# Optimization experiments

Measured on AMD Instinct MI355X. Metric: run time of the kernel, lower is better.

## Reference

```python
import jax, jax.numpy as jnp
import numpy as np
from itertools import product

SPATIAL1 = (41, 1600, 1408)  # (z,y,x) = grid[::-1] + [1,0,0]
NUM_BATCH = 2
BN_EPS = 1e-3

# ---------- numpy rulebook construction (spconv-style, done once on host) ----------

def _encode(c, shape):
    D, H, W = [int(v) for v in shape]
    return ((c[:, 0].astype(np.int64) * D + c[:, 1]) * H + c[:, 2]) * W + c[:, 3]

def _lookup(skeys, order, cand):
    pos = np.clip(np.searchsorted(skeys, cand), 0, len(skeys) - 1)
    hit = skeys[pos] == cand
    return hit, order[pos]

def _pad_rb(pairs, n_in, n_out):
    P = max(max(len(a) for a, _ in pairs), 1)
    K = len(pairs)
    ii = np.full((K, P), n_in, np.int32)   # sentinel -> zero feature row
    oo = np.full((K, P), n_out, np.int32)  # sentinel -> dummy output row
    for k, (a, b) in enumerate(pairs):
        ii[k, :len(a)] = a
        oo[k, :len(b)] = b
    return ii, oo

def _subm_rb(coords, shape):
    # SubMConv3d k=3 p=1 s=1: output sites == input sites
    N = len(coords)
    keys = _encode(coords, shape)
    order = np.argsort(keys); skeys = keys[order]
    dims = np.array(shape)
    pairs = []
    for off in product((-1, 0, 1), repeat=3):
        nb = coords[:, 1:] + np.array(off)
        ok = (nb >= 0).all(1) & (nb < dims).all(1)
        oid = np.nonzero(ok)[0]
        cand = _encode(np.concatenate([coords[ok, :1], nb[ok]], 1), shape)
        hit, iid = _lookup(skeys, order, cand)
        pairs.append((iid[hit].astype(np.int32), oid[hit].astype(np.int32)))
    return _pad_rb(pairs, N, N)

def _down_rb(coords, in_shape, ks, st, pd):
    # SparseConv3d: output site active iff any kernel tap hits an active input
    dims = np.array(in_shape); ks = np.array(ks); st = np.array(st); pd = np.array(pd)
    out_shape = (dims + 2 * pd - ks) // st + 1
    offs = list(product(*[range(int(k)) for k in ks]))
    outs = []
    for off in offs:
        o = coords[:, 1:] + pd - np.array(off)
        ok = (o % st == 0).all(1)
        od = o // st
        ok &= (od >= 0).all(1) & (od < out_shape).all(1)
        outs.append(np.concatenate([coords[ok, :1], od[ok]], 1))
    out_coords = np.unique(np.concatenate(outs, 0), axis=0)
    keys = _encode(coords, in_shape)
    order = np.argsort(keys); skeys = keys[order]
    pairs = []
    for off in offs:
        ic = out_coords[:, 1:] * st - pd + np.array(off)
        ok = (ic >= 0).all(1) & (ic < dims).all(1)
        oid = np.nonzero(ok)[0]
        cand = _encode(np.concatenate([out_coords[ok, :1], ic[ok]], 1), in_shape)
        hit, iid = _lookup(skeys, order, cand)
        pairs.append((iid[hit].astype(np.int32), oid[hit].astype(np.int32)))
    ii, oo = _pad_rb(pairs, len(coords), len(out_coords))
    return ii, oo, out_coords, tuple(int(v) for v in out_shape)

def _gen_coords(rng):
    # clustered LiDAR-like active voxels (surfaces -> local density)
    D, H, W = SPATIAL1
    per = []
    for b in range(NUM_BATCH):
        centers = rng.integers([3, 30, 30], [D - 4, H - 31, W - 31], size=(600, 3))
        pts = centers[:, None, :] + rng.integers(-3, 4, size=(600, 60, 3))
        pts = np.clip(pts.reshape(-1, 3), 0, np.array([D - 1, H - 1, W - 1]))
        uniq = np.unique(pts, axis=0)
        per.append(np.concatenate([np.full((len(uniq), 1), b, np.int64), uniq], 1))
    return np.concatenate(per, 0)

CHANS = [(27, 4, 16), (27, 16, 16), (27, 16, 32), (27, 32, 32), (27, 32, 32),
         (27, 32, 64), (27, 64, 64), (27, 64, 64), (27, 64, 64), (27, 64, 64),
         (27, 64, 64), (3, 64, 128)]

def setup_inputs() -> dict:
    rng = np.random.default_rng(0)
    coords = _gen_coords(rng)  # (N,4) [b,z,y,x]
    N = len(coords)
    s1i, s1o = _subm_rb(coords, SPATIAL1)
    d2i, d2o, c2, s2 = _down_rb(coords, SPATIAL1, (3, 3, 3), (2, 2, 2), (1, 1, 1))
    s2i, s2o = _subm_rb(c2, s2)
    d3i, d3o, c3, s3 = _down_rb(c2, s2, (3, 3, 3), (2, 2, 2), (1, 1, 1))
    s3i, s3o = _subm_rb(c3, s3)
    d4i, d4o, c4, s4 = _down_rb(c3, s3, (3, 3, 3), (2, 2, 2), (0, 1, 1))
    s4i, s4o = _subm_rb(c4, s4)
    oi, oo, c5, s5 = _down_rb(c4, s4, (3, 1, 1), (2, 1, 1), (0, 0, 0))

    key = jax.random.key(0)
    ks = jax.random.split(key, 40)
    inp = {}
    for i, (K, ci, co) in enumerate(CHANS):
        inp[f"w{i}"] = (jax.random.normal(ks[i], (K, ci, co), jnp.float32)
                         / np.sqrt(K * ci)).astype(jnp.float32)
        kb = jax.random.split(ks[12 + i], 4)
        inp[f"bn{i}"] = jnp.stack([
            jax.random.uniform(kb[0], (co,)) + 0.5,   # gamma
            jax.random.normal(kb[1], (co,)) * 0.1,    # beta
            jax.random.normal(kb[2], (co,)) * 0.1,    # running mean
            jax.random.uniform(kb[3], (co,)) + 0.5,   # running var
        ]).astype(jnp.float32)
    inp["voxels"] = jax.random.normal(ks[30], (N, 5, 4), jnp.float32)
    inp["voxel_num_points"] = jax.random.randint(ks[31], (N,), 0, 6).astype(jnp.int32)
    for name, arr in [("subm1_in", s1i), ("subm1_out", s1o), ("down2_in", d2i),
                      ("down2_out", d2o), ("subm2_in", s2i), ("subm2_out", s2o),
                      ("down3_in", d3i), ("down3_out", d3o), ("subm3_in", s3i),
                      ("subm3_out", s3o), ("down4_in", d4i), ("down4_out", d4o),
                      ("subm4_in", s4i), ("subm4_out", s4o), ("out_in", oi),
                      ("out_out", oo)]:
        inp[name] = jnp.asarray(arr)
    inp["batch_idx"] = jnp.asarray(c5[:, 0].astype(np.int32))
    inp["n2"] = len(c2); inp["n3"] = len(c3); inp["n4"] = len(c4); inp["n5"] = len(c5)
    inp["n_batch"] = NUM_BATCH
    return inp

# ---------- jax forward ----------

def _sconv(feats, w, in_idx, out_idx, n_out):
    # gather -> per-kernel-offset GEMM -> scatter-add (spconv implicit GEMM)
    fpad = jnp.concatenate([feats, jnp.zeros((1, feats.shape[1]), feats.dtype)], 0)
    g = fpad[in_idx]                                  # (K,P,Cin)
    contrib = jnp.einsum('kpi,kio->kpo', g, w)        # (K,P,Cout)
    out = jnp.zeros((n_out + 1, w.shape[2]), feats.dtype)
    return out.at[out_idx].add(contrib)[:n_out]

def _bnrelu(x, bn):
    g, b, m, v = bn  # eval-mode BatchNorm1d, eps=1e-3
    return jax.nn.relu((x - m) * jax.lax.rsqrt(v + BN_EPS) * g + b)

def reference(voxels, voxel_num_points, w0, w1, w2, w3, w4, w5, w6, w7, w8, w9,
              w10, w11, bn0, bn1, bn2, bn3, bn4, bn5, bn6, bn7, bn8, bn9, bn10,
              bn11, subm1_in, subm1_out, down2_in, down2_out, subm2_in, subm2_out,
              down3_in, down3_out, subm3_in, subm3_out, down4_in, down4_out,
              subm4_in, subm4_out, out_in, out_out, batch_idx, n2, n3, n4, n5,
              n_batch):
    # mean-VFE: average point features per voxel
    denom = jnp.maximum(voxel_num_points.astype(voxels.dtype), 1.0)[:, None]
    x = voxels.sum(1) / denom                              # (N,4)
    n1 = x.shape[0]
    x = _bnrelu(_sconv(x, w0, subm1_in, subm1_out, n1), bn0)   # conv_input
    x = _bnrelu(_sconv(x, w1, subm1_in, subm1_out, n1), bn1)   # conv1
    x = _bnrelu(_sconv(x, w2, down2_in, down2_out, n2), bn2)   # conv2 (s2)
    x = _bnrelu(_sconv(x, w3, subm2_in, subm2_out, n2), bn3)
    x = _bnrelu(_sconv(x, w4, subm2_in, subm2_out, n2), bn4)
    x = _bnrelu(_sconv(x, w5, down3_in, down3_out, n3), bn5)   # conv3 (s2)
    x = _bnrelu(_sconv(x, w6, subm3_in, subm3_out, n3), bn6)
    x = _bnrelu(_sconv(x, w7, subm3_in, subm3_out, n3), bn7)
    x = _bnrelu(_sconv(x, w8, down4_in, down4_out, n4), bn8)   # conv4 (s2)
    x = _bnrelu(_sconv(x, w9, subm4_in, subm4_out, n4), bn9)
    x = _bnrelu(_sconv(x, w10, subm4_in, subm4_out, n4), bn10)
    x = _bnrelu(_sconv(x, w11, out_in, out_out, n5), bn11)     # conv_out
    # dc_feats: per-sample global max pool over active voxels (== max_pool1d)
    dc = jax.ops.segment_max(x, batch_idx, num_segments=n_batch)
    return dc
```

## Files before the change

kernel.cpp:

```cpp
#include <hip/hip_runtime.h>

#define TPB 256
typedef unsigned short u16;
typedef __attribute__((ext_vector_type(8))) short short8v;
typedef __attribute__((ext_vector_type(4))) float f32x4;

__device__ __forceinline__ u16 f2bf(float x) {
    unsigned u = __float_as_uint(x);
    return (u16)((u + 0x7FFFu + ((u >> 16) & 1u)) >> 16);
}
__device__ __forceinline__ float bf2f(u16 h) {
    return __uint_as_float(((unsigned)h) << 16);
}

template<int CS>
__device__ __forceinline__ int swzc(int r, int c) {
    constexpr int PH = (CS == 8) ? 0 : 1;
    return c ^ ((r >> PH) & (CS - 1));
}

__device__ __forceinline__ int xcd_swz(int bid, int nwg) {
    int q = nwg >> 3, r = nwg & 7;
    int x = bid & 7, idx = bid >> 3;
    return (x < r ? x * (q + 1) : r * (q + 1) + (x - r) * q) + idx;
}

__device__ __forceinline__ void gld16(const u16* g, u16* l) {
    __builtin_amdgcn_global_load_lds(
        (const __attribute__((address_space(1))) void*)g,
        (__attribute__((address_space(3))) void*)l, 16, 0, 0);
}

__global__ void vfe_kernel(const float* __restrict__ voxels,
                           const int* __restrict__ nump,
                           float* __restrict__ x, int N) {
    int i = blockIdx.x * blockDim.x + threadIdx.x;
    if (i >= N * 4) return;
    int n = i >> 2, c = i & 3;
    const float* v = voxels + (long)n * 20 + c;
    float s = v[0] + v[4] + v[8] + v[12] + v[16];
    x[i] = s / fmaxf((float)nump[n], 1.0f);
}

__global__ void inv_build_kernel(const int* __restrict__ rb_in,
                                 const int* __restrict__ rb_out,
                                 int* __restrict__ inv,
                                 int KP, int P, int K, int n_in) {
    int t = blockIdx.x * blockDim.x + threadIdx.x;
    if (t >= KP) return;
    int ii = rb_in[t];
    if (ii == n_in) return;
    int k = t / P;
    inv[(long)rb_out[t] * K + k] = ii;
}

struct WPE { const float* w; u16* oh; u16* ol; int K, ci, co, total; };
struct WPA { WPE e[9]; };
__global__ void wprep_kernel(WPA a, int grand) {
    int t = blockIdx.x * blockDim.x + threadIdx.x;
    if (t >= grand) return;
    #pragma unroll
    for (int i = 0; i < 9; ++i) {
        if (t < a.e[i].total) {
            const WPE& E = a.e[i];
            int cc = E.ci * E.co;
            int k = t / cc, r = t % cc, c = r / E.co, o = r % E.co;
            float x = E.w[t];
            u16 h = f2bf(x);
            float lf = x - bf2f(h);
            int cs = E.ci >> 3, ph = (cs == 8) ? 0 : 1;
            int ch = c >> 3, e = c & 7;
            int sch = ch ^ ((o >> ph) & (cs - 1));
            long d = ((long)k * E.co + o) * E.ci + sch * 8 + e;
            E.oh[d] = h; E.ol[d] = f2bf(lf);
            return;
        }
        t -= a.e[i].total;
    }
}

__global__ void wprep_paired_kernel(const float* __restrict__ w,
                                    u16* __restrict__ oh, u16* __restrict__ ol,
                                    int co, int total) {
    int t = blockIdx.x * blockDim.x + threadIdx.x;
    if (t >= total) return;
    int p = t / (co * 32);
    int rem = t % (co * 32);
    int o = rem / 32, ci = rem % 32;
    int tap = 2 * p + (ci >> 4);
    float x = (tap < 27) ? w[((long)tap * 16 + (ci & 15)) * co + o] : 0.f;
    u16 h = f2bf(x);
    float lf = x - bf2f(h);
    int ch = ci >> 3, e = ci & 7;
    int sch = ch ^ ((o >> 1) & 3);
    long d = ((long)p * co + o) * 32 + sch * 8 + e;
    oh[d] = h; ol[d] = f2bf(lf);
}

template<int CO, int K>
__global__ __launch_bounds__(256)
void dconv4_kernel(const float* __restrict__ feats,
                   const float* __restrict__ w,
                   const float* __restrict__ bn,
                   const int* __restrict__ inv,
                   u16* __restrict__ oh, u16* __restrict__ ol,
                   int n_out) {
    constexpr int OG = CO / 4;
    __shared__ float sW[K * 4 * CO];
    for (int i = threadIdx.x; i < K * 4 * CO; i += 256) sW[i] = w[i];
    __syncthreads();
    long t = (long)blockIdx.x * 256 + threadIdx.x;
    int row = (int)(t / OG), og = (int)(t % OG);
    if (row >= n_out) return;
    float a0 = 0.f, a1 = 0.f, a2 = 0.f, a3 = 0.f;
    for (int k = 0; k < K; ++k) {
        int idx = inv[(long)row * K + k];
        if (idx < 0) continue;
        float4 av = *(const float4*)(feats + (long)idx * 4);
        const float* wk = sW + k * 4 * CO + og * 4;
        #pragma unroll
        for (int ci = 0; ci < 4; ++ci) {
            float a = (&av.x)[ci];
            a0 = fmaf(a, wk[ci * CO + 0], a0);
            a1 = fmaf(a, wk[ci * CO + 1], a1);
            a2 = fmaf(a, wk[ci * CO + 2], a2);
            a3 = fmaf(a, wk[ci * CO + 3], a3);
        }
    }
    float4 g = *(const float4*)(bn + og * 4);
    float4 b = *(const float4*)(bn + CO + og * 4);
    float4 m = *(const float4*)(bn + 2 * CO + og * 4);
    float4 v = *(const float4*)(bn + 3 * CO + og * 4);
    float o4[4];
    o4[0] = fmaxf((a0 - m.x) * rsqrtf(v.x + 1e-3f) * g.x + b.x, 0.f);
    o4[1] = fmaxf((a1 - m.y) * rsqrtf(v.y + 1e-3f) * g.y + b.y, 0.f);
    o4[2] = fmaxf((a2 - m.z) * rsqrtf(v.z + 1e-3f) * g.z + b.z, 0.f);
    o4[3] = fmaxf((a3 - m.w) * rsqrtf(v.w + 1e-3f) * g.w + b.w, 0.f);
    long base = (long)row * CO + og * 4;
    #pragma unroll
    for (int c = 0; c < 4; ++c) {
        u16 h = f2bf(o4[c]);
        oh[base + c] = h;
        ol[base + c] = f2bf(o4[c] - bf2f(h));
    }
}

template<int CI, int CO, int KPt, int KT, bool PAIRED, bool DBUF, int EPI>
__global__ __launch_bounds__(256, 4)
void mconv_kernel(const u16* __restrict__ fh, const u16* __restrict__ fl,
                  const u16* __restrict__ wh, const u16* __restrict__ wl,
                  const int* __restrict__ inv,
                  const u16* __restrict__ zpage,
                  float* __restrict__ part, long slab_elems,
                  const float* __restrict__ bn,
                  u16* __restrict__ oh, u16* __restrict__ ol,
                  float* __restrict__ outf,
                  int n_out, int kpb) {
    constexpr int CS  = CI / 8;
    constexpr int LCS = (CS == 8) ? 3 : 2;
    constexpr int PH  = (CS == 8) ? 0 : 1;
    constexpr int KS  = CI / 32;
    constexpr int WC  = (CO >= 32) ? 2 : 1;
    constexpr int MT  = (WC == 2) ? 2 : 1;
    constexpr int NTW = CO / (16 * WC);
    constexpr int ASL = 64 * CS;
    constexpr int BSL = CO * CS;
    constexpr int AIT = (ASL + 255) / 256;
    constexpr int BIT = (BSL + 255) / 256;
    constexpr int NB  = DBUF ? 2 : 1;

    __shared__ __align__(16) u16 sAh[NB][64 * CI];
    __shared__ __align__(16) u16 sAl[NB][64 * CI];
    __shared__ __align__(16) u16 sBh[NB][CO * CI];
    __shared__ __align__(16) u16 sBl[NB][CO * CI];
    __shared__ int sI[64 * KT];

    const int t = threadIdx.x;
    const int bx = xcd_swz(blockIdx.x, gridDim.x);
    const int brow = bx * 64;
    const int kbeg = blockIdx.y * kpb;
    const int kend = (kbeg + kpb < KPt) ? (kbeg + kpb) : KPt;

    const int lane = t & 63, wid = t >> 6;
    const int wr = wid / WC, wc = wid % WC;
    const int frow = lane & 15;
    const int fch  = lane >> 4;

    {
        long base = (long)brow * KT, lim = (long)n_out * KT;
        for (int i = t; i < 64 * KT; i += 256)
            sI[i] = (base + i < lim) ? inv[base + i] : -1;
    }

    f32x4 acc[MT][NTW];
    #pragma unroll
    for (int mt = 0; mt < MT; ++mt)
        #pragma unroll
        for (int nt = 0; nt < NTW; ++nt) {
            acc[mt][nt][0] = 0.f; acc[mt][nt][1] = 0.f;
            acc[mt][nt][2] = 0.f; acc[mt][nt][3] = 0.f;
        }

    auto stage = [&](int b, int k) {
        #pragma unroll
        for (int s = 0; s < AIT; ++s) {
            int slot = s * 256 + t;
            if (ASL % 256 == 0 || slot < ASL) {
                int r = slot >> LCS, cc = slot & (CS - 1);
                int c = cc ^ ((r >> PH) & (CS - 1));
                const u16 *srcH, *srcL;
                if (PAIRED) {
                    int tap = 2 * k + (c >> 1);
                    int idx = (tap < KT) ? sI[r * KT + tap] : -1;
                    srcH = (idx >= 0) ? fh + (long)idx * 16 + (c & 1) * 8 : zpage;
                    srcL = (idx >= 0) ? fl + (long)idx * 16 + (c & 1) * 8 : zpage;
                } else {
                    int idx = sI[r * KT + k];
                    srcH = (idx >= 0) ? fh + (long)idx * CI + c * 8 : zpage;
                    srcL = (idx >= 0) ? fl + (long)idx * CI + c * 8 : zpage;
                }
                gld16(srcH, sAh[b] + (s * 256 + wid * 64) * 8);
                gld16(srcL, sAl[b] + (s * 256 + wid * 64) * 8);
            }
        }
        const u16* gbh = wh + (long)k * CO * CI;
        const u16* gbl = wl + (long)k * CO * CI;
        #pragma unroll
        for (int s = 0; s < BIT; ++s) {
            int slot = s * 256 + t;
            if (BSL % 256 == 0 || slot < BSL) {
                gld16(gbh + (long)slot * 8, sBh[b] + (s * 256 + wid * 64) * 8);
                gld16(gbl + (long)slot * 8, sBl[b] + (s * 256 + wid * 64) * 8);
            }
        }
    };
    auto compute = [&](int b) {
        #pragma unroll
        for (int ks = 0; ks < KS; ++ks) {
            int c = ks * 4 + fch;
            short8v ah[MT], al[MT];
            #pragma unroll
            for (int mt = 0; mt < MT; ++mt) {
                int r = wr * (MT * 16) + mt * 16 + frow;
                int o = r * CI + swzc<CS>(r, c) * 8;
                ah[mt] = *(const short8v*)(sAh[b] + o);
                al[mt] = *(const short8v*)(sAl[b] + o);
            }
            #pragma unroll
            for (int nt = 0; nt < NTW; ++nt) {
                int col = wc * (CO / WC) + nt * 16 + frow;
                int o = col * CI + swzc<CS>(col, c) * 8;
                short8v bh = *(const short8v*)(sBh[b] + o);
                short8v bl = *(const short8v*)(sBl[b] + o);
                #pragma unroll
                for (int mt = 0; mt < MT; ++mt) {
                    acc[mt][nt] = __builtin_amdgcn_mfma_f32_16x16x32_bf16(ah[mt], bh, acc[mt][nt], 0, 0, 0);
                    acc[mt][nt] = __builtin_amdgcn_mfma_f32_16x16x32_bf16(ah[mt], bl, acc[mt][nt], 0, 0, 0);
                    acc[mt][nt] = __builtin_amdgcn_mfma_f32_16x16x32_bf16(al[mt], bh, acc[mt][nt], 0, 0, 0);
                }
            }
        }
    };

    __syncthreads();
    if (DBUF) {
        stage(0, kbeg);
        int cur = 0;
        for (int k = kbeg; k < kend; ++k) {
            __syncthreads();
            if (k + 1 < kend) stage(cur ^ 1, k + 1);
            compute(cur);
            cur ^= 1;
        }
    } else {
        for (int k = kbeg; k < kend; ++k) {
            stage(0, k);
            __syncthreads();
            compute(0);
            if (k + 1 < kend) __syncthreads();
        }
    }

    if constexpr (EPI == 0) {
        float* dst = part + (long)blockIdx.y * slab_elems;
        #pragma unroll
        for (int mt = 0; mt < MT; ++mt) {
            int orow0 = brow + wr * (MT * 16) + mt * 16 + (lane >> 4) * 4;
            #pragma unroll
            for (int nt = 0; nt < NTW; ++nt) {
                int ocol = wc * (CO / WC) + nt * 16 + (lane & 15);
                #pragma unroll
                for (int j = 0; j < 4; ++j) {
                    int r = orow0 + j;
                    if (r < n_out) dst[(long)r * CO + ocol] = acc[mt][nt][j];
                }
            }
        }
    } else {
        #pragma unroll
        for (int mt = 0; mt < MT; ++mt) {
            int orow0 = brow + wr * (MT * 16) + mt * 16 + (lane >> 4) * 4;
            #pragma unroll
            for (int nt = 0; nt < NTW; ++nt) {
                int ocol = wc * (CO / WC) + nt * 16 + (lane & 15);
                float g = bn[ocol], bb = bn[CO + ocol];
                float m = bn[2 * CO + ocol], vv = bn[3 * CO + ocol];
                float sc = rsqrtf(vv + 1e-3f) * g;
                #pragma unroll
                for (int j = 0; j < 4; ++j) {
                    int r = orow0 + j;
                    if (r < n_out) {
                        float yv = fmaxf((acc[mt][nt][j] - m) * sc + bb, 0.f);
                        if constexpr (EPI == 1) {
                            u16 h = f2bf(yv);
                            oh[(long)r * CO + ocol] = h;
                            ol[(long)r * CO + ocol] = f2bf(yv - bf2f(h));
                        } else {
                            outf[(long)r * CO + ocol] = yv;
                        }
                    }
                }
            }
        }
    }
}

template<bool EMIT16>
__global__ void reduce_bnrelu_kernel(const float* __restrict__ part, long stride,
                                     int ys, const float* __restrict__ bn, int co,
                                     float* __restrict__ outf,
                                     u16* __restrict__ oh, u16* __restrict__ ol,
                                     long total) {
    long t = (long)blockIdx.x * blockDim.x + threadIdx.x;
    if (t >= total) return;
    float s = 0.f;
    for (int y = 0; y < ys; ++y) s += part[(long)y * stride + t];
    int o = (int)(t % co);
    float g = bn[o], b = bn[co + o], m = bn[2 * co + o], v = bn[3 * co + o];
    float yv = fmaxf((s - m) * rsqrtf(v + 1e-3f) * g + b, 0.f);
    if (EMIT16) {
        u16 h = f2bf(yv);
        oh[t] = h;
        ol[t] = f2bf(yv - bf2f(h));
    } else {
        outf[t] = yv;
    }
}

__global__ void segmax_kernel(const float* __restrict__ x,
                              const int* __restrict__ bidx,
                              float* __restrict__ out, int rows, int nb) {
    __shared__ float sM[8 * 128];
    for (int i = threadIdx.x; i < nb * 128; i += 256) sM[i] = 0.f;
    __syncthreads();
    int c = threadIdx.x & 127;
    int sub = threadIdx.x >> 7;
    for (int r = blockIdx.x * 2 + sub; r < rows; r += gridDim.x * 2) {
        float v = x[(long)r * 128 + c];
        int b = bidx[r];
        atomicMax((int*)&sM[b * 128 + c], __float_as_int(v));
    }
    __syncthreads();
    for (int i = threadIdx.x; i < nb * 128; i += 256)
        atomicMax((int*)out + i, __float_as_int(sM[i]));
}

extern "C" void kernel_launch(void* const* d_in, const int* in_sizes, int n_in,
                              void* d_out, int out_size, void* d_ws, size_t ws_size,
                              hipStream_t stream) {
    (void)n_in;
    const float* voxels = (const float*)d_in[24];
    const int*   nump   = (const int*)d_in[25];
    const int N  = in_sizes[25];
    const int n2 = in_sizes[30] / 27;
    const int n3 = in_sizes[34] / 27;
    const int n4 = in_sizes[38] / 27;
    const int n5 = in_sizes[42];

    struct L { int wi, rb, K, ci, co, nin, nout; };
    const L layers[12] = {
        {0,  26, 27,  4,  16, N,  N }, {1,  26, 27, 16,  16, N,  N },
        {2,  28, 27, 16,  32, N,  n2}, {3,  30, 27, 32,  32, n2, n2},
        {4,  30, 27, 32,  32, n2, n2}, {5,  32, 27, 32,  64, n2, n3},
        {6,  34, 27, 64,  64, n3, n3}, {7,  34, 27, 64,  64, n3, n3},
        {8,  36, 27, 64,  64, n3, n4}, {9,  38, 27, 64,  64, n4, n4},
        {10, 38, 27, 64,  64, n4, n4}, {11, 40,  3, 64, 128, n4, n5},
    };
    struct RBD { int rb, K, nin, nout; };
    const RBD rbs[8] = {
        {26, 27, N,  N }, {28, 27, N,  n2}, {30, 27, n2, n2}, {32, 27, n2, n3},
        {34, 27, n3, n3}, {36, 27, n3, n4}, {38, 27, n4, n4}, {40, 3,  n4, n5},
    };
    const int invmap[12] = {0, 0, 1, 2, 2, 3, 4, 4, 5, 6, 6, 7};

    size_t feat_elems = (size_t)N * 4, wt_elems = 0, arena_elems = 0;
    for (int i = 0; i < 12; ++i) {
        size_t fe = (size_t)layers[i].nout * layers[i].co;
        if (fe > feat_elems) feat_elems = fe;
        if (i >= 3) wt_elems += (size_t)layers[i].K * layers[i].ci * layers[i].co;
    }
    for (int r = 0; r < 8; ++r) arena_elems += (size_t)rbs[r].nout * rbs[r].K;
    const size_t wp1_elems = 14 * 32 * 16;
    const size_t wp2_elems = 14 * 32 * 32;
    auto al = [](size_t x) { return (x + 255) & ~(size_t)255; };
    char* p = (char*)d_ws;
    u16*   zpage = (u16*)p; p += 256;
    int*   inv_arena = (int*)p; p += al(arena_elems * 4);
    float* bufA = (float*)p; p += al(feat_elems * 4);
    u16* ph[2]; u16* pl[2];
    ph[0] = (u16*)p; p += al(feat_elems * 2);
    pl[0] = (u16*)p; p += al(feat_elems * 2);
    ph[1] = (u16*)p; p += al(feat_elems * 2);
    pl[1] = (u16*)p; p += al(feat_elems * 2);
    u16* wth = (u16*)p; p += al(wt_elems * 2);
    u16* wtl = (u16*)p; p += al(wt_elems * 2);
    u16* wp1h = (u16*)p; p += al(wp1_elems * 2);
    u16* wp1l = (u16*)p; p += al(wp1_elems * 2);
    u16* wp2h = (u16*)p; p += al(wp2_elems * 2);
    u16* wp2l = (u16*)p; p += al(wp2_elems * 2);
    float* slab = (float*)p;
    size_t slab_budget = ws_size - (size_t)((char*)slab - (char*)d_ws);

    hipMemsetAsync(zpage, 0, 256, stream);

    int* invs[8];
    {
        size_t off = 0;
        for (int r = 0; r < 8; ++r) { invs[r] = inv_arena + off; off += (size_t)rbs[r].nout * rbs[r].K; }
        hipMemsetAsync(inv_arena, 0xFF, arena_elems * sizeof(int), stream);
        for (int r = 0; r < 8; ++r) {
            const int* rin  = (const int*)d_in[rbs[r].rb];
            const int* rout = (const int*)d_in[rbs[r].rb + 1];
            int P  = in_sizes[rbs[r].rb] / rbs[r].K;
            int KP = rbs[r].K * P;
            inv_build_kernel<<<dim3((KP + TPB - 1) / TPB), dim3(TPB), 0, stream>>>(
                rin, rout, invs[r], KP, P, rbs[r].K, rbs[r].nin);
        }
    }

    {
        long tot = (long)N * 4;
        vfe_kernel<<<dim3((unsigned)((tot + TPB - 1) / TPB)), dim3(TPB), 0, stream>>>(
            voxels, nump, bufA, N);
    }

    size_t woff[9];
    {
        WPA wa;
        size_t off = 0;
        for (int i = 0; i < 9; ++i) {
            const L& l = layers[i + 3];
            woff[i] = off;
            wa.e[i].w  = (const float*)d_in[2 * l.wi];
            wa.e[i].oh = wth + off;
            wa.e[i].ol = wtl + off;
            wa.e[i].K = l.K; wa.e[i].ci = l.ci; wa.e[i].co = l.co;
            wa.e[i].total = l.K * l.ci * l.co;
            off += (size_t)wa.e[i].total;
        }
        int grand = (int)off;
        wprep_kernel<<<dim3((grand + TPB - 1) / TPB), dim3(TPB), 0, stream>>>(wa, grand);
        wprep_paired_kernel<<<dim3(((int)wp1_elems + TPB - 1) / TPB), dim3(TPB), 0, stream>>>(
            (const float*)d_in[2], wp1h, wp1l, 16, (int)wp1_elems);
        wprep_paired_kernel<<<dim3(((int)wp2_elems + TPB - 1) / TPB), dim3(TPB), 0, stream>>>(
            (const float*)d_in[4], wp2h, wp2l, 32, (int)wp2_elems);
    }

    {
        const L& l = layers[0];
        long tot = (long)l.nout * 4;
        dconv4_kernel<16, 27><<<dim3((unsigned)((tot + 255) / 256)), 256, 0, stream>>>(
            bufA, (const float*)d_in[0], (const float*)d_in[1], invs[0],
            ph[0], pl[0], l.nout);
    }

    int cset = 0;
    for (int i = 1; i < 12; ++i) {
        const L& l = layers[i];
        const int* invp = invs[invmap[i]];
        unsigned blocks = (unsigned)((l.nout + 63) / 64);
        int KPv = (i <= 2) ? 14 : l.K;
        int ysmax = (KPv == 14) ? 9 : ((KPv == 27) ? 27 : 3);
        size_t per = (size_t)l.nout * l.co * 4;
        int ys = 1;
        while (ys < ysmax && blocks * (unsigned)ys < 768) ys *= 3;
        if (ys > ysmax) ys = ysmax;
        while (ys > 1 && (size_t)ys * per > slab_budget) ys /= 3;
        int kpb = (KPv + ys - 1) / ys;
        long slab_elems = (long)l.nout * l.co;
        dim3 grid(blocks, (unsigned)ys);
        const float* bn = (const float*)d_in[2 * l.wi + 1];
        const u16* fh = ph[cset];
        const u16* fl = pl[cset];
        const u16* whp = (i >= 3) ? wth + woff[i - 3] : nullptr;
        const u16* wlp = (i >= 3) ? wtl + woff[i - 3] : nullptr;

        #define MCONV(CI_, CO_, KP_, KT_, PRD_, WH_, WL_)                              \
            do {                                                                       \
                if (ys == 1 && i < 11)                                                 \
                    mconv_kernel<CI_, CO_, KP_, KT_, PRD_, true, 1><<<grid, 256, 0, stream>>>( \
                        fh, fl, WH_, WL_, invp, zpage, nullptr, 0, bn,                 \
                        ph[cset ^ 1], pl[cset ^ 1], nullptr, l.nout, kpb);             \
                else if (ys == 1)                                                      \
                    mconv_kernel<CI_, CO_, KP_, KT_, PRD_, true, 2><<<grid, 256, 0, stream>>>( \
                        fh, fl, WH_, WL_, invp, zpage, nullptr, 0, bn,                 \
                        nullptr, nullptr, bufA, l.nout, kpb);                          \
                else if (kpb >= 2)                                                     \
                    mconv_kernel<CI_, CO_, KP_, KT_, PRD_, true, 0><<<grid, 256, 0, stream>>>( \
                        fh, fl, WH_, WL_, invp, zpage, slab, slab_elems, bn,           \
                        nullptr, nullptr, nullptr, l.nout, kpb);                       \
                else                                                                   \
                    mconv_kernel<CI_, CO_, KP_, KT_, PRD_, false, 0><<<grid, 256, 0, stream>>>( \
                        fh, fl, WH_, WL_, invp, zpage, slab, slab_elems, bn,           \
                        nullptr, nullptr, nullptr, l.nout, kpb);                       \
            } while (0)

        switch (i) {
        case 1:          MCONV(32, 16, 14, 27, true,  wp1h, wp1l); break;
        case 2:          MCONV(32, 32, 14, 27, true,  wp2h, wp2l); break;
        case 3: case 4:  MCONV(32, 32, 27, 27, false, whp, wlp);   break;
        case 5:          MCONV(32, 64, 27, 27, false, whp, wlp);   break;
        case 11:         MCONV(64, 128, 3, 3,  false, whp, wlp);   break;
        default:         MCONV(64, 64, 27, 27, false, whp, wlp);   break;
        }
        #undef MCONV

        if (ys == 1) {
            if (i < 11) cset ^= 1;
        } else {
            long total = (long)l.nout * l.co;
            unsigned rblocks = (unsigned)((total + TPB - 1) / TPB);
            if (i < 11) {
                reduce_bnrelu_kernel<true><<<dim3(rblocks), dim3(TPB), 0, stream>>>(
                    slab, slab_elems, ys, bn, l.co,
                    nullptr, ph[cset ^ 1], pl[cset ^ 1], total);
                cset ^= 1;
            } else {
                reduce_bnrelu_kernel<false><<<dim3(rblocks), dim3(TPB), 0, stream>>>(
                    slab, slab_elems, ys, bn, l.co, bufA, nullptr, nullptr, total);
            }
        }
    }

    hipMemsetAsync(d_out, 0, (size_t)out_size * sizeof(float), stream);
    const int* bidx = (const int*)d_in[42];
    int nb = out_size / 128;
    segmax_kernel<<<dim3(128), dim3(256), 0, stream>>>(bufA, bidx, (float*)d_out, n5, nb);
}
```

Baseline: 482.6 us.

## Drop double-buffered staging and shared index cache in sparse conv kernel

Removes the double-buffered shared-memory pipeline and the per-block shared copy of the rulebook indices. Each tap is now staged, synced and computed in sequence, and the gather reads indices straight from global memory. The aim is to halve LDS use so more blocks fit per CU and to drop the up-front index preload. The cost is that loads for the next tap no longer overlap compute, and index reads become dependent global loads on the gather path.

```diff
diff --git a/kernel.cpp b/kernel.cpp
--- a/kernel.cpp
+++ b/kernel.cpp
@@ -145,7 +145,7 @@
     }
 }
 
-template<int CI, int CO, int KPt, int KT, bool PAIRED, bool DBUF, int EPI>
+template<int CI, int CO, int KPt, int KT, bool PAIRED, int EPI>
 __global__ __launch_bounds__(256, 4)
 void mconv_kernel(const u16* __restrict__ fh, const u16* __restrict__ fl,
                   const u16* __restrict__ wh, const u16* __restrict__ wl,
@@ -167,13 +167,11 @@
     constexpr int BSL = CO * CS;
     constexpr int AIT = (ASL + 255) / 256;
     constexpr int BIT = (BSL + 255) / 256;
-    constexpr int NB  = DBUF ? 2 : 1;
-
-    __shared__ __align__(16) u16 sAh[NB][64 * CI];
-    __shared__ __align__(16) u16 sAl[NB][64 * CI];
-    __shared__ __align__(16) u16 sBh[NB][CO * CI];
-    __shared__ __align__(16) u16 sBl[NB][CO * CI];
-    __shared__ int sI[64 * KT];
+
+    __shared__ __align__(16) u16 sAh[64 * CI];
+    __shared__ __align__(16) u16 sAl[64 * CI];
+    __shared__ __align__(16) u16 sBh[CO * CI];
+    __shared__ __align__(16) u16 sBl[CO * CI];
 
     const int t = threadIdx.x;
     const int bx = xcd_swz(blockIdx.x, gridDim.x);
@@ -186,12 +184,6 @@
     const int frow = lane & 15;
     const int fch  = lane >> 4;
 
-    {
-        long base = (long)brow * KT, lim = (long)n_out * KT;
-        for (int i = t; i < 64 * KT; i += 256)
-            sI[i] = (base + i < lim) ? inv[base + i] : -1;
-    }
-
     f32x4 acc[MT][NTW];
     #pragma unroll
     for (int mt = 0; mt < MT; ++mt)
@@ -201,26 +193,28 @@
             acc[mt][nt][2] = 0.f; acc[mt][nt][3] = 0.f;
         }
 
-    auto stage = [&](int b, int k) {
+    auto stage = [&](int k) {
         #pragma unroll
         for (int s = 0; s < AIT; ++s) {
             int slot = s * 256 + t;
             if (ASL % 256 == 0 || slot < ASL) {
                 int r = slot >> LCS, cc = slot & (CS - 1);
                 int c = cc ^ ((r >> PH) & (CS - 1));
+                int grow = brow + r;
                 const u16 *srcH, *srcL;
                 if (PAIRED) {
                     int tap = 2 * k + (c >> 1);
-                    int idx = (tap < KT) ? sI[r * KT + tap] : -1;
+                    int idx = (grow < n_out && tap < KT)
+                              ? inv[(long)grow * KT + tap] : -1;
                     srcH = (idx >= 0) ? fh + (long)idx * 16 + (c & 1) * 8 : zpage;
                     srcL = (idx >= 0) ? fl + (long)idx * 16 + (c & 1) * 8 : zpage;
                 } else {
-                    int idx = sI[r * KT + k];
+                    int idx = (grow < n_out) ? inv[(long)grow * KT + k] : -1;
                     srcH = (idx >= 0) ? fh + (long)idx * CI + c * 8 : zpage;
                     srcL = (idx >= 0) ? fl + (long)idx * CI + c * 8 : zpage;
                 }
-                gld16(srcH, sAh[b] + (s * 256 + wid * 64) * 8);
-                gld16(srcL, sAl[b] + (s * 256 + wid * 64) * 8);
+                gld16(srcH, sAh + (s * 256 + wid * 64) * 8);
+                gld16(srcL, sAl + (s * 256 + wid * 64) * 8);
             }
         }
         const u16* gbh = wh + (long)k * CO * CI;
@@ -229,12 +223,12 @@
         for (int s = 0; s < BIT; ++s) {
             int slot = s * 256 + t;
             if (BSL % 256 == 0 || slot < BSL) {
-                gld16(gbh + (long)slot * 8, sBh[b] + (s * 256 + wid * 64) * 8);
-                gld16(gbl + (long)slot * 8, sBl[b] + (s * 256 + wid * 64) * 8);
+                gld16(gbh + (long)slot * 8, sBh + (s * 256 + wid * 64) * 8);
+                gld16(gbl + (long)slot * 8, sBl + (s * 256 + wid * 64) * 8);
             }
         }
     };
-    auto compute = [&](int b) {
+    auto compute = [&]() {
         #pragma unroll
         for (int ks = 0; ks < KS; ++ks) {
             int c = ks * 4 + fch;
@@ -243,15 +237,15 @@
             for (int mt = 0; mt < MT; ++mt) {
                 int r = wr * (MT * 16) + mt * 16 + frow;
                 int o = r * CI + swzc<CS>(r, c) * 8;
-                ah[mt] = *(const short8v*)(sAh[b] + o);
-                al[mt] = *(const short8v*)(sAl[b] + o);
+                ah[mt] = *(const short8v*)(sAh + o);
+                al[mt] = *(const short8v*)(sAl + o);
             }
             #pragma unroll
             for (int nt = 0; nt < NTW; ++nt) {
                 int col = wc * (CO / WC) + nt * 16 + frow;
                 int o = col * CI + swzc<CS>(col, c) * 8;
-                short8v bh = *(const short8v*)(sBh[b] + o);
-                short8v bl = *(const short8v*)(sBl[b] + o);
+                short8v bh = *(const short8v*)(sBh + o);
+                short8v bl = *(const short8v*)(sBl + o);
                 #pragma unroll
                 for (int mt = 0; mt < MT; ++mt) {
                     acc[mt][nt] = __builtin_amdgcn_mfma_f32_16x16x32_bf16(ah[mt], bh, acc[mt][nt], 0, 0, 0);
@@ -262,23 +256,11 @@
         }
     };
 
-    __syncthreads();
-    if (DBUF) {
-        stage(0, kbeg);
-        int cur = 0;
-        for (int k = kbeg; k < kend; ++k) {
-            __syncthreads();
-            if (k + 1 < kend) stage(cur ^ 1, k + 1);
-            compute(cur);
-            cur ^= 1;
-        }
-    } else {
-        for (int k = kbeg; k < kend; ++k) {
-            stage(0, k);
-            __syncthreads();
-            compute(0);
-            if (k + 1 < kend) __syncthreads();
-        }
+    for (int k = kbeg; k < kend; ++k) {
+        stage(k);
+        __syncthreads();
+        compute();
+        if (k + 1 < kend) __syncthreads();
     }
 
     if constexpr (EPI == 0) {
@@ -498,19 +480,15 @@
         #define MCONV(CI_, CO_, KP_, KT_, PRD_, WH_, WL_)                              \
             do {                                                                       \
                 if (ys == 1 && i < 11)                                                 \
-                    mconv_kernel<CI_, CO_, KP_, KT_, PRD_, true, 1><<<grid, 256, 0, stream>>>( \
+                    mconv_kernel<CI_, CO_, KP_, KT_, PRD_, 1><<<grid, 256, 0, stream>>>( \
                         fh, fl, WH_, WL_, invp, zpage, nullptr, 0, bn,                 \
                         ph[cset ^ 1], pl[cset ^ 1], nullptr, l.nout, kpb);             \
                 else if (ys == 1)                                                      \
-                    mconv_kernel<CI_, CO_, KP_, KT_, PRD_, true, 2><<<grid, 256, 0, stream>>>( \
+                    mconv_kernel<CI_, CO_, KP_, KT_, PRD_, 2><<<grid, 256, 0, stream>>>( \
                         fh, fl, WH_, WL_, invp, zpage, nullptr, 0, bn,                 \
                         nullptr, nullptr, bufA, l.nout, kpb);                          \
-                else if (kpb >= 2)                                                     \
-                    mconv_kernel<CI_, CO_, KP_, KT_, PRD_, true, 0><<<grid, 256, 0, stream>>>( \
-                        fh, fl, WH_, WL_, invp, zpage, slab, slab_elems, bn,           \
-                        nullptr, nullptr, nullptr, l.nout, kpb);                       \
                 else                                                                   \
-                    mconv_kernel<CI_, CO_, KP_, KT_, PRD_, false, 0><<<grid, 256, 0, stream>>>( \
+                    mconv_kernel<CI_, CO_, KP_, KT_, PRD_, 0><<<grid, 256, 0, stream>>>( \
                         fh, fl, WH_, WL_, invp, zpage, slab, slab_elems, bn,           \
                         nullptr, nullptr, nullptr, l.nout, kpb);                       \
             } while (0)
```

Measured after the change: 432.2 us. 10.4% less time.
